# Optimization experiments

Hardware: AMD Instinct MI355X
Metric: run time of the kernel (lower is better)

## Reference

```python
import jax, jax.numpy as jnp
import numpy as np

B, N, K = 4, 32768, 16          # batch, nodes, neighbors per node
CIN, H, COUT, P = 32, 32, 32, 3  # in/hidden/out channels, phy_dim


def setup_inputs() -> dict:
    key = jax.random.key(0)
    ks = jax.random.split(key, 8)
    x = jax.random.normal(ks[0], (B, CIN, N), jnp.float32)
    grid = jax.random.uniform(ks[1], (B, N, P), jnp.float32)
    grid_weight = jax.random.uniform(ks[2], (B, N), jnp.float32)
    edge_src = jax.random.randint(ks[3], (B, N, K), 0, N)
    edge_dst = jax.random.randint(ks[4], (B, N, K), 0, N)
    # fc1: Linear(CIN, H); fc2: Linear(H, COUT)
    W1 = jax.random.normal(ks[5], (H, CIN), jnp.float32) * (1.0 / np.sqrt(CIN))
    b1 = jnp.zeros((H,), jnp.float32)
    W2 = jax.random.normal(ks[6], (COUT, H), jnp.float32) * (1.0 / np.sqrt(H))
    b2 = jnp.zeros((COUT,), jnp.float32)
    # learned Gaussian bandwidth, positive, broadcast over hidden channels
    baseweight = jax.random.uniform(ks[7], (H,), jnp.float32, minval=0.5, maxval=2.0)
    return {"x": x, "grid": grid, "grid_weight": grid_weight,
            "edge_src": edge_src, "edge_dst": edge_dst,
            "W1": W1, "b1": b1, "W2": W2, "b2": b2, "baseweight": baseweight}


def reference(x, grid, grid_weight, edge_src, edge_dst, W1, b1, W2, b2, baseweight):
    bsz, _, n = x.shape
    phy_dim = grid.shape[-1]
    # fc1 on (bsz, N, CIN)
    h = jnp.einsum('bcn,hc->bnh', x, W1) + b1              # (B, N, H)
    hidden = h.shape[-1]
    # flatten batch with per-batch node offsets (edges are intra-batch)
    off = (jnp.arange(bsz, dtype=edge_src.dtype) * n).reshape(bsz, 1, 1)
    es = (edge_src + off).reshape(-1)                       # (E,)
    ed = (edge_dst + off).reshape(-1)                       # (E,)
    grid_f = grid.reshape(-1, phy_dim)                      # (B*N, P)
    gw_f = grid_weight.reshape(-1)                          # (B*N,)
    h_f = h.reshape(-1, hidden)                             # (B*N, H)
    # squared pairwise distance per edge; exp(-w*sqrt(d2)**2) == exp(-w*d2)
    d2 = jnp.sum((grid_f[es] - grid_f[ed]) ** 2, axis=1)    # (E,)
    gauss = jnp.sqrt((baseweight / jnp.pi) ** phy_dim) * jnp.exp(-baseweight * d2[:, None])  # (E, H)
    src = gauss * h_f[es] * gw_f[es][:, None]               # (E, H)
    out = jax.ops.segment_sum(src, ed, num_segments=bsz * n)  # (B*N, H)
    out = out.reshape(bsz, n, hidden)
    out = jnp.einsum('bnh,oh->bno', out, W2) + b2           # (B, N, COUT)
    return out.transpose(0, 2, 1)                           # (B, COUT, N)
```

## Files before the change

kernel.cpp:

```cpp
#include <hip/hip_runtime.h>
#include <math.h>

constexpr int B    = 4;
constexpr int N    = 32768;
constexpr int K    = 16;
constexpr int CIN  = 32;
constexpr int H    = 32;
constexpr int COUT = 32;
constexpr int NODES = B * N;
constexpr int E      = B * N * K;

constexpr int BPB        = 512;
constexpr int NBUCKETS   = B * BPB;
constexpr int BUCKET_CAP = 2048;
constexpr int BIN_EDGES  = 8192;
constexpr int BIN_BLOCKS = E / BIN_EDGES;
constexpr int BIN_THREADS = 1024;

__global__ __launch_bounds__(256) void k_fc1(const float* __restrict__ x,
                                             const float* __restrict__ grid_weight,
                                             const float* __restrict__ W1,
                                             const float* __restrict__ b1,
                                             const float* __restrict__ baseweight,
                                             float* __restrict__ hh)
{
    __shared__ float sW1[H * CIN];
    __shared__ float sb1[H];
    __shared__ float scoef[H];
    const int tid = threadIdx.x;
    for (int i = tid; i < H * CIN; i += 256) sW1[i] = W1[i];
    if (tid < H) {
        sb1[tid] = b1[tid];
        float t = baseweight[tid] * (float)(1.0 / M_PI);
        scoef[tid] = t * sqrtf(t);
    }
    __syncthreads();

    const int node = blockIdx.x * 256 + tid;
    const int b = node >> 15;
    const int n = node & (N - 1);
    const float* xb = x + (size_t)b * CIN * N + n;

    float acc[H];
#pragma unroll
    for (int h = 0; h < H; ++h) acc[h] = sb1[h];
#pragma unroll
    for (int c = 0; c < CIN; ++c) {
        float xv = xb[(size_t)c * N];
#pragma unroll
        for (int h = 0; h < H; ++h) acc[h] = fmaf(xv, sW1[h * CIN + c], acc[h]);
    }
    const float gw = grid_weight[node];

    float4* dst = (float4*)(hh + (size_t)node * H);
#pragma unroll
    for (int i = 0; i < H / 4; ++i) {
        float4 v;
        v.x = acc[4 * i + 0] * gw * scoef[4 * i + 0];
        v.y = acc[4 * i + 1] * gw * scoef[4 * i + 1];
        v.z = acc[4 * i + 2] * gw * scoef[4 * i + 2];
        v.w = acc[4 * i + 3] * gw * scoef[4 * i + 3];
        dst[i] = v;
    }
}

__global__ __launch_bounds__(BIN_THREADS) void k_bin(const int* __restrict__ esrc,
                                                     const int* __restrict__ edst,
                                                     int* __restrict__ gcur,
                                                     unsigned* __restrict__ gbucket)
{
    __shared__ int hist[BPB];
    __shared__ int lbase[BPB];
    __shared__ int cur[BPB];
    __shared__ int gbase[BPB];
    __shared__ int sc[256];
    __shared__ unsigned staged[BIN_EDGES];

    const int tid = threadIdx.x;
    const int e0  = blockIdx.x * BIN_EDGES;
    const int batch = blockIdx.x >> 6;

    for (int i = tid; i < BPB; i += BIN_THREADS) hist[i] = 0;
    __syncthreads();

#pragma unroll
    for (int i = 0; i < BIN_EDGES / BIN_THREADS; ++i) {
        const int d = edst[e0 + i * BIN_THREADS + tid];
        atomicAdd(&hist[d >> 6], 1);
    }
    __syncthreads();

    int h0 = 0, h1 = 0;
    if (tid < 256) {
        h0 = hist[2 * tid];
        h1 = hist[2 * tid + 1];
        sc[tid] = h0 + h1;
    }
    __syncthreads();
    for (int off = 1; off < 256; off <<= 1) {
        int v = 0;
        if (tid < 256 && tid >= off) v = sc[tid - off];
        __syncthreads();
        if (tid < 256) sc[tid] += v;
        __syncthreads();
    }
    if (tid < 256) {
        const int pairExcl = sc[tid] - (h0 + h1);
        lbase[2 * tid]     = pairExcl;
        lbase[2 * tid + 1] = pairExcl + h0;
        cur[2 * tid]       = pairExcl;
        cur[2 * tid + 1]   = pairExcl + h0;
    }
    __syncthreads();

    if (tid < BPB) gbase[tid] = atomicAdd(&gcur[batch * BPB + tid], hist[tid]);

#pragma unroll
    for (int i = 0; i < BIN_EDGES / BIN_THREADS; ++i) {
        const int idx = e0 + i * BIN_THREADS + tid;
        const int d = edst[idx];
        const int s = esrc[idx];
        const int pos = atomicAdd(&cur[d >> 6], 1);
        staged[pos] = ((unsigned)d << 16) | (unsigned)s;
    }
    __syncthreads();

    unsigned* gb_batch = gbucket + (size_t)batch * BPB * BUCKET_CAP;
#pragma unroll
    for (int i = 0; i < BIN_EDGES / BIN_THREADS; ++i) {
        const int idx = i * BIN_THREADS + tid;
        const unsigned v = staged[idx];
        const int bkt = (int)(v >> 22);
        const int p = gbase[bkt] + (idx - lbase[bkt]);
        if (p < BUCKET_CAP) gb_batch[(size_t)bkt * BUCKET_CAP + p] = v;
    }
}

__global__ __launch_bounds__(256) void k_gather2(const float* __restrict__ grid,
                                                 const float* __restrict__ baseweight,
                                                 const float* __restrict__ hh,
                                                 const unsigned* __restrict__ gbucket,
                                                 const int* __restrict__ gcur,
                                                 const float* __restrict__ W2,
                                                 const float* __restrict__ b2,
                                                 float* __restrict__ out)
{
    __shared__ float sW2[COUT][H + 1];
    __shared__ float sb2[COUT];
    __shared__ float sbw[H];
    __shared__ float tmp[8][H + 1];
    __shared__ float stage[64][COUT + 1];
    __shared__ int hist64[64];
    __shared__ int base64[64];
    __shared__ int cur64[64];
    __shared__ unsigned short srt[BUCKET_CAP];

    const int tid = threadIdx.x;
    for (int i = tid; i < COUT * H; i += 256) sW2[i >> 5][i & 31] = W2[i];
    if (tid < COUT) sb2[tid] = b2[tid];
    if (tid < H)    sbw[tid] = baseweight[tid];
    if (tid < 64)   hist64[tid] = 0;
    __syncthreads();

    const int bi    = blockIdx.x;
    const int batch = (bi & 7) >> 1;
    const int bloc  = ((bi >> 3) << 1) | (bi & 1);
    const int gb    = batch * BPB + bloc;

    const int bb    = batch * N;
    const int n0    = bloc * 64;

    const int cnt = min(gcur[gb], BUCKET_CAP);
    const unsigned* bp = gbucket + (size_t)gb * BUCKET_CAP;

    unsigned ent[BUCKET_CAP / 256];
#pragma unroll
    for (int j = 0; j < BUCKET_CAP / 256; ++j) {
        const int i = j * 256 + tid;
        if (i < cnt) {
            ent[j] = bp[i];
            atomicAdd(&hist64[(ent[j] >> 16) & 63], 1);
        }
    }
    __syncthreads();

    if (tid < 64) base64[tid] = hist64[tid];
    __syncthreads();
    for (int off = 1; off < 64; off <<= 1) {
        int v = 0;
        if (tid < 64 && tid >= off) v = base64[tid - off];
        __syncthreads();
        if (tid < 64) base64[tid] += v;
        __syncthreads();
    }
    if (tid < 64) {
        base64[tid] -= hist64[tid];
        cur64[tid]   = base64[tid];
    }
    __syncthreads();

#pragma unroll
    for (int j = 0; j < BUCKET_CAP / 256; ++j) {
        const int i = j * 256 + tid;
        if (i < cnt) {
            const int pos = atomicAdd(&cur64[(ent[j] >> 16) & 63], 1);
            srt[pos] = (unsigned short)(ent[j] & 0xFFFFu);
        }
    }
    __syncthreads();

    const int g    = tid >> 5;
    const int lane = tid & 31;
    const float bwl = sbw[lane];

#pragma unroll
    for (int r = 0; r < 8; ++r) {
        const int nl  = g * 8 + r;
        const int d   = bb + n0 + nl;
        const int off = base64[nl];
        const int cn  = hist64[nl];
        const float gx = grid[d * 3 + 0];
        const float gy = grid[d * 3 + 1];
        const float gz = grid[d * 3 + 2];

        float acc = 0.0f;
        for (int base = 0; base < cn; base += 32) {
            const int m = min(32, cn - base);

            int   s_l  = 0;
            float d2_l = 0.0f;
            if (lane < m) {
                s_l = bb + (int)srt[off + base + lane];
                const float dx = grid[s_l * 3 + 0] - gx;
                const float dy = grid[s_l * 3 + 1] - gy;
                const float dz = grid[s_l * 3 + 2] - gz;
                d2_l = dx * dx + dy * dy + dz * dz;
            }

            int i = 0;
            for (; i + 4 <= m; i += 4) {
                const int s0 = __shfl(s_l, i + 0, 32);
                const int s1 = __shfl(s_l, i + 1, 32);
                const int s2 = __shfl(s_l, i + 2, 32);
                const int s3 = __shfl(s_l, i + 3, 32);
                const float w0 = __shfl(d2_l, i + 0, 32);
                const float w1 = __shfl(d2_l, i + 1, 32);
                const float w2 = __shfl(d2_l, i + 2, 32);
                const float w3 = __shfl(d2_l, i + 3, 32);
                const float f0 = hh[(size_t)s0 * H + lane];
                const float f1 = hh[(size_t)s1 * H + lane];
                const float f2 = hh[(size_t)s2 * H + lane];
                const float f3 = hh[(size_t)s3 * H + lane];
                acc = fmaf(__expf(-bwl * w0), f0, acc);
                acc = fmaf(__expf(-bwl * w1), f1, acc);
                acc = fmaf(__expf(-bwl * w2), f2, acc);
                acc = fmaf(__expf(-bwl * w3), f3, acc);
            }
            for (; i < m; ++i) {
                const int   s = __shfl(s_l, i, 32);
                const float w = __shfl(d2_l, i, 32);
                acc = fmaf(__expf(-bwl * w), hh[(size_t)s * H + lane], acc);
            }
        }

        tmp[g][lane] = acc;
        float o_val = sb2[lane];
#pragma unroll
        for (int h = 0; h < H; ++h)
            o_val = fmaf(tmp[g][h], sW2[lane][h], o_val);
        stage[nl][lane] = o_val;
    }
    __syncthreads();

    float* ob = out + (size_t)batch * COUT * N + n0;
#pragma unroll
    for (int i = 0; i < 8; ++i) {
        const int flat = i * 256 + tid;
        const int o = flat >> 6;
        const int j = flat & 63;
        ob[(size_t)o * N + j] = stage[j][o];
    }
}

extern "C" void kernel_launch(void* const* d_in, const int* in_sizes, int n_in,
                              void* d_out, int out_size, void* d_ws, size_t ws_size,
                              hipStream_t stream)
{
    const float* x    = (const float*)d_in[0];
    const float* grid = (const float*)d_in[1];
    const float* gw   = (const float*)d_in[2];
    const int*   es   = (const int*)d_in[3];
    const int*   ed   = (const int*)d_in[4];
    const float* W1   = (const float*)d_in[5];
    const float* b1   = (const float*)d_in[6];
    const float* W2   = (const float*)d_in[7];
    const float* b2   = (const float*)d_in[8];
    const float* bw   = (const float*)d_in[9];
    float* out = (float*)d_out;

    char* w = (char*)d_ws;
    float*    hh      = (float*)(w);
    unsigned* gbucket = (unsigned*)(w + (size_t)NODES * H * 4);
    int*      gcur    = (int*)(w + (size_t)NODES * H * 4
                                 + (size_t)NBUCKETS * BUCKET_CAP * 4);

    hipMemsetAsync(gcur, 0, (size_t)NBUCKETS * sizeof(int), stream);

    k_fc1<<<NODES / 256, 256, 0, stream>>>(x, gw, W1, b1, bw, hh);
    k_bin<<<BIN_BLOCKS, BIN_THREADS, 0, stream>>>(es, ed, gcur, gbucket);
    k_gather2<<<NBUCKETS, 256, 0, stream>>>(grid, bw, hh, gbucket, gcur,
                                            W2, b2, out);
}
```

Before: 181.9 us.

## Replace per-bucket counting sort with LDS atomic accumulation in gather

```diff
diff --git a/kernel.cpp b/kernel.cpp
--- a/kernel.cpp
+++ b/kernel.cpp
@@ -16,6 +16,7 @@
 constexpr int BIN_EDGES  = 8192;
 constexpr int BIN_BLOCKS = E / BIN_EDGES;
 constexpr int BIN_THREADS = 1024;
+constexpr int EPT = BIN_EDGES / BIN_THREADS;
 
 __global__ __launch_bounds__(256) void k_fc1(const float* __restrict__ x,
                                              const float* __restrict__ grid_weight,
@@ -83,10 +84,11 @@
     for (int i = tid; i < BPB; i += BIN_THREADS) hist[i] = 0;
     __syncthreads();
 
-#pragma unroll
-    for (int i = 0; i < BIN_EDGES / BIN_THREADS; ++i) {
-        const int d = edst[e0 + i * BIN_THREADS + tid];
-        atomicAdd(&hist[d >> 6], 1);
+    int ed_r[EPT];
+#pragma unroll
+    for (int i = 0; i < EPT; ++i) {
+        ed_r[i] = edst[e0 + i * BIN_THREADS + tid];
+        atomicAdd(&hist[ed_r[i] >> 6], 1);
     }
     __syncthreads();
 
@@ -116,10 +118,9 @@
     if (tid < BPB) gbase[tid] = atomicAdd(&gcur[batch * BPB + tid], hist[tid]);
 
 #pragma unroll
-    for (int i = 0; i < BIN_EDGES / BIN_THREADS; ++i) {
-        const int idx = e0 + i * BIN_THREADS + tid;
-        const int d = edst[idx];
-        const int s = esrc[idx];
+    for (int i = 0; i < EPT; ++i) {
+        const int s = esrc[e0 + i * BIN_THREADS + tid];
+        const int d = ed_r[i];
         const int pos = atomicAdd(&cur[d >> 6], 1);
         staged[pos] = ((unsigned)d << 16) | (unsigned)s;
     }
@@ -127,7 +128,7 @@
 
     unsigned* gb_batch = gbucket + (size_t)batch * BPB * BUCKET_CAP;
 #pragma unroll
-    for (int i = 0; i < BIN_EDGES / BIN_THREADS; ++i) {
+    for (int i = 0; i < EPT; ++i) {
         const int idx = i * BIN_THREADS + tid;
         const unsigned v = staged[idx];
         const int bkt = (int)(v >> 22);
@@ -136,7 +137,7 @@
     }
 }
 
-__global__ __launch_bounds__(256) void k_gather2(const float* __restrict__ grid,
+__global__ __launch_bounds__(256) void k_gather3(const float* __restrict__ grid,
                                                  const float* __restrict__ baseweight,
                                                  const float* __restrict__ hh,
                                                  const unsigned* __restrict__ gbucket,
@@ -148,126 +149,83 @@
     __shared__ float sW2[COUT][H + 1];
     __shared__ float sb2[COUT];
     __shared__ float sbw[H];
-    __shared__ float tmp[8][H + 1];
+    __shared__ float sgrid[64 * 3];
+    __shared__ float acc[64][H + 1];
     __shared__ float stage[64][COUT + 1];
-    __shared__ int hist64[64];
-    __shared__ int base64[64];
-    __shared__ int cur64[64];
-    __shared__ unsigned short srt[BUCKET_CAP];
 
     const int tid = threadIdx.x;
     for (int i = tid; i < COUT * H; i += 256) sW2[i >> 5][i & 31] = W2[i];
     if (tid < COUT) sb2[tid] = b2[tid];
     if (tid < H)    sbw[tid] = baseweight[tid];
-    if (tid < 64)   hist64[tid] = 0;
-    __syncthreads();
+    for (int i = tid; i < 64 * (H + 1); i += 256) ((float*)acc)[i] = 0.0f;
 
     const int bi    = blockIdx.x;
     const int batch = (bi & 7) >> 1;
     const int bloc  = ((bi >> 3) << 1) | (bi & 1);
     const int gb    = batch * BPB + bloc;
-
     const int bb    = batch * N;
     const int n0    = bloc * 64;
 
+    if (tid < 192) sgrid[tid] = grid[((size_t)(bb + n0)) * 3 + tid];
+    __syncthreads();
+
     const int cnt = min(gcur[gb], BUCKET_CAP);
     const unsigned* bp = gbucket + (size_t)gb * BUCKET_CAP;
-
-    unsigned ent[BUCKET_CAP / 256];
-#pragma unroll
-    for (int j = 0; j < BUCKET_CAP / 256; ++j) {
-        const int i = j * 256 + tid;
-        if (i < cnt) {
-            ent[j] = bp[i];
-            atomicAdd(&hist64[(ent[j] >> 16) & 63], 1);
-        }
-    }
-    __syncthreads();
-
-    if (tid < 64) base64[tid] = hist64[tid];
-    __syncthreads();
-    for (int off = 1; off < 64; off <<= 1) {
-        int v = 0;
-        if (tid < 64 && tid >= off) v = base64[tid - off];
-        __syncthreads();
-        if (tid < 64) base64[tid] += v;
-        __syncthreads();
-    }
-    if (tid < 64) {
-        base64[tid] -= hist64[tid];
-        cur64[tid]   = base64[tid];
-    }
-    __syncthreads();
-
-#pragma unroll
-    for (int j = 0; j < BUCKET_CAP / 256; ++j) {
-        const int i = j * 256 + tid;
-        if (i < cnt) {
-            const int pos = atomicAdd(&cur64[(ent[j] >> 16) & 63], 1);
-            srt[pos] = (unsigned short)(ent[j] & 0xFFFFu);
-        }
-    }
-    __syncthreads();
 
     const int g    = tid >> 5;
     const int lane = tid & 31;
     const float bwl = sbw[lane];
 
+    for (int c = g; c * 32 < cnt; c += 8) {
+        const int m = min(32, cnt - c * 32);
+
+        unsigned v_l = 0;
+        float d2_l = 0.0f;
+        if (lane < m) {
+            v_l = bp[c * 32 + lane];
+            const int s  = bb + (int)(v_l & 0xFFFFu);
+            const int dl = (int)((v_l >> 16) & 63u);
+            const float dx = grid[s * 3 + 0] - sgrid[dl * 3 + 0];
+            const float dy = grid[s * 3 + 1] - sgrid[dl * 3 + 1];
+            const float dz = grid[s * 3 + 2] - sgrid[dl * 3 + 2];
+            d2_l = dx * dx + dy * dy + dz * dz;
+        }
+
+        int i = 0;
+        for (; i + 4 <= m; i += 4) {
+            const unsigned v0 = __shfl(v_l, i + 0, 32);
+            const unsigned v1 = __shfl(v_l, i + 1, 32);
+            const unsigned v2 = __shfl(v_l, i + 2, 32);
+            const unsigned v3 = __shfl(v_l, i + 3, 32);
+            const float w0 = __shfl(d2_l, i + 0, 32);
+            const float w1 = __shfl(d2_l, i + 1, 32);
+            const float w2 = __shfl(d2_l, i + 2, 32);
+            const float w3 = __shfl(d2_l, i + 3, 32);
+            const float f0 = hh[(size_t)(bb + (v0 & 0xFFFFu)) * H + lane];
+            const float f1 = hh[(size_t)(bb + (v1 & 0xFFFFu)) * H + lane];
+            const float f2 = hh[(size_t)(bb + (v2 & 0xFFFFu)) * H + lane];
+            const float f3 = hh[(size_t)(bb + (v3 & 0xFFFFu)) * H + lane];
+            atomicAdd(&acc[(v0 >> 16) & 63][lane], __expf(-bwl * w0) * f0);
+            atomicAdd(&acc[(v1 >> 16) & 63][lane], __expf(-bwl * w1) * f1);
+            atomicAdd(&acc[(v2 >> 16) & 63][lane], __expf(-bwl * w2) * f2);
+            atomicAdd(&acc[(v3 >> 16) & 63][lane], __expf(-bwl * w3) * f3);
+        }
+        for (; i < m; ++i) {
+            const unsigned v = __shfl(v_l, i, 32);
+            const float    w = __shfl(d2_l, i, 32);
+            const float    f = hh[(size_t)(bb + (v & 0xFFFFu)) * H + lane];
+            atomicAdd(&acc[(v >> 16) & 63][lane], __expf(-bwl * w) * f);
+        }
+    }
+    __syncthreads();
+
 #pragma unroll
     for (int r = 0; r < 8; ++r) {
-        const int nl  = g * 8 + r;
-        const int d   = bb + n0 + nl;
-        const int off = base64[nl];
-        const int cn  = hist64[nl];
-        const float gx = grid[d * 3 + 0];
-        const float gy = grid[d * 3 + 1];
-        const float gz = grid[d * 3 + 2];
-
-        float acc = 0.0f;
-        for (int base = 0; base < cn; base += 32) {
-            const int m = min(32, cn - base);
-
-            int   s_l  = 0;
-            float d2_l = 0.0f;
-            if (lane < m) {
-                s_l = bb + (int)srt[off + base + lane];
-                const float dx = grid[s_l * 3 + 0] - gx;
-                const float dy = grid[s_l * 3 + 1] - gy;
-                const float dz = grid[s_l * 3 + 2] - gz;
-                d2_l = dx * dx + dy * dy + dz * dz;
-            }
-
-            int i = 0;
-            for (; i + 4 <= m; i += 4) {
-                const int s0 = __shfl(s_l, i + 0, 32);
-                const int s1 = __shfl(s_l, i + 1, 32);
-                const int s2 = __shfl(s_l, i + 2, 32);
-                const int s3 = __shfl(s_l, i + 3, 32);
-                const float w0 = __shfl(d2_l, i + 0, 32);
-                const float w1 = __shfl(d2_l, i + 1, 32);
-                const float w2 = __shfl(d2_l, i + 2, 32);
-                const float w3 = __shfl(d2_l, i + 3, 32);
-                const float f0 = hh[(size_t)s0 * H + lane];
-                const float f1 = hh[(size_t)s1 * H + lane];
-                const float f2 = hh[(size_t)s2 * H + lane];
-                const float f3 = hh[(size_t)s3 * H + lane];
-                acc = fmaf(__expf(-bwl * w0), f0, acc);
-                acc = fmaf(__expf(-bwl * w1), f1, acc);
-                acc = fmaf(__expf(-bwl * w2), f2, acc);
-                acc = fmaf(__expf(-bwl * w3), f3, acc);
-            }
-            for (; i < m; ++i) {
-                const int   s = __shfl(s_l, i, 32);
-                const float w = __shfl(d2_l, i, 32);
-                acc = fmaf(__expf(-bwl * w), hh[(size_t)s * H + lane], acc);
-            }
-        }
-
-        tmp[g][lane] = acc;
+        const int nl = g * 8 + r;
         float o_val = sb2[lane];
 #pragma unroll
         for (int h = 0; h < H; ++h)
-            o_val = fmaf(tmp[g][h], sW2[lane][h], o_val);
+            o_val = fmaf(acc[nl][h], sW2[lane][h], o_val);
         stage[nl][lane] = o_val;
     }
     __syncthreads();
@@ -308,6 +266,6 @@
 
     k_fc1<<<NODES / 256, 256, 0, stream>>>(x, gw, W1, b1, bw, hh);
     k_bin<<<BIN_BLOCKS, BIN_THREADS, 0, stream>>>(es, ed, gcur, gbucket);
-    k_gather2<<<NBUCKETS, 256, 0, stream>>>(grid, bw, hh, gbucket, gcur,
+    k_gather3<<<NBUCKETS, 256, 0, stream>>>(grid, bw, hh, gbucket, gcur,
                                             W2, b2, out);
 }
```

New measurement: 502.6 us. +176.2%, slower.
